# Kernel optimization log

Hardware: AMD Instinct MI355X
Metric: run time of the kernel (lower is better)

The kernel has to match this reference:

```python
import jax
import jax.numpy as jnp
from jax import lax
import numpy as np

EPS = 1e-5
CLASS_COUNT = 1000

# conv specs: (out_c, in_c, k, pool_stride)
_SPECS = [(8, 1, 11, 1), (32, 8, 7, 2), (64, 32, 5, 2), (64, 64, 5, 2), (128, 64, 5, 2), (128, 128, 3, 2)]


def _maxpool3(x, stride):
    return lax.reduce_window(x, -jnp.inf, lax.max, (1, 1, 3, 3), (1, 1, stride, stride), 'VALID')


def _block(x, w, gamma, beta, pool_stride):
    # tanh soft-binarized weights (mode=1, w=1)
    wq = jnp.tanh(w)
    y = lax.conv_general_dilated(x, wq, (1, 1), 'VALID', dimension_numbers=('NCHW', 'OIHW', 'NCHW'))
    y = _maxpool3(y, pool_stride)
    # BatchNorm2d in training mode: batch statistics over (N,H,W), biased var
    mu = jnp.mean(y, axis=(0, 2, 3), keepdims=True)
    var = jnp.var(y, axis=(0, 2, 3), keepdims=True)
    y = (y - mu) * lax.rsqrt(var + EPS)
    y = y * gamma.reshape(1, -1, 1, 1) + beta.reshape(1, -1, 1, 1)
    # tanh soft-binarized activation (mode=1, w=1)
    return jnp.tanh(y)


def setup_inputs() -> dict:
    key = jax.random.key(0)
    keys = jax.random.split(key, 8)
    inp = {'x': jax.random.normal(keys[0], (128, 1, 227, 227), dtype=jnp.float32)}
    for i, (oc, ic, k, _) in enumerate(_SPECS):
        fan_in = ic * k * k
        inp[f'w{i+1}'] = jax.random.normal(keys[i + 1], (oc, ic, k, k), dtype=jnp.float32) / np.sqrt(fan_in)
        inp[f'g{i+1}'] = jnp.ones((oc,), dtype=jnp.float32)
        inp[f'b{i+1}'] = jnp.zeros((oc,), dtype=jnp.float32)
    inp['wl'] = jax.random.normal(keys[7], (CLASS_COUNT, 512), dtype=jnp.float32) / np.sqrt(512.0)
    return inp


def reference(x, w1, w2, w3, w4, w5, w6, g1, g2, g3, g4, g5, g6,
              b1, b2, b3, b4, b5, b6, wl):
    ws = (w1, w2, w3, w4, w5, w6)
    gs = (g1, g2, g3, g4, g5, g6)
    bs = (b1, b2, b3, b4, b5, b6)
    for i, (_, _, _, ps) in enumerate(_SPECS):
        x = _block(x, ws[i], gs[i], bs[i], ps)
    # flatten -> BinaryLinear (tanh-binarized weight, no bias)
    x = x.reshape(x.shape[0], -1)  # [B, 512]
    return x @ jnp.tanh(wl).T  # [B, classCount]
```

## Files before the change

### kernel.cpp

```cpp
#include <hip/hip_runtime.h>
#include <hip/hip_bf16.h>
#include <hip/hip_fp16.h>

using bf16 = __hip_bfloat16;
using f16  = _Float16;
using f16x8 = __attribute__((ext_vector_type(8))) _Float16;
using f32x4  = __attribute__((ext_vector_type(4))) float;
typedef unsigned long long u64;

__device__ __forceinline__ float b2f(bf16 v){ return __bfloat162float(v); }
__device__ __forceinline__ bf16 f2b(float v){ return __float2bfloat16(v); }
__device__ __forceinline__ float ldf(const float* p){ return *p; }
__device__ __forceinline__ float ldf(const bf16* p){ return b2f(*p); }
__device__ __forceinline__ float ldf(const __half* p){ return __half2float(*p); }
__device__ __forceinline__ void stf(float* p, float v){ *p = v; }
__device__ __forceinline__ void stf(bf16* p, float v){ *p = f2b(v); }
__device__ __forceinline__ void stf(__half* p, float v){ *p = __float2half(v); }

__device__ __forceinline__ float ftanh(float x){
    float t = __builtin_amdgcn_exp2f(x * 2.8853900817779268f);
    return 1.0f - 2.0f * __builtin_amdgcn_rcpf(t + 1.0f);
}

__device__ __forceinline__ float ld_any(const void* p, int i, int isBf16)
{
    return isBf16 ? b2f(((const bf16*)p)[i]) : ((const float*)p)[i];
}

__device__ __forceinline__ int det_bf(const void* g)
{
    return (*(const unsigned*)g == 0x3F803F80u) ? 1 : 0;
}

__device__ __forceinline__ void bn_pr(const float* __restrict__ sums,
                                      const void* __restrict__ g,
                                      const void* __restrict__ b,
                                      int bf, int C, float inv, int c,
                                      float& sc, float& sh)
{
    float mean = sums[c] * inv;
    float var  = sums[C + c] * inv - mean * mean;
    float rstd = rsqrtf(fmaxf(var, 0.f) + 1e-5f);
    sc = ld_any(g, c, bf) * rstd;
    sh = ld_any(b, c, bf) - mean * sc;
}

__global__ __launch_bounds__(256)
void prep_all(const void* __restrict__ w1, const void* __restrict__ w6,
              const void* __restrict__ wlw, const void* __restrict__ w2,
              const void* __restrict__ w3, const void* __restrict__ w4,
              const void* __restrict__ w5, const void* __restrict__ g1,
              float* __restrict__ wq0, float* __restrict__ wq5,
              float* __restrict__ wlqT, __half* __restrict__ wpk,
              __half* __restrict__ wpk3, __half* __restrict__ wpk4,
              __half* __restrict__ wpk5, int* __restrict__ flag)
{
    const int bf = det_bf(g1);
    const int b = blockIdx.x, t = threadIdx.x;
    if (b == 0 && t == 0) *flag = bf;
    if (b < 4) {
        int i = b * 256 + t;
        if (i < 968) wq0[i] = tanhf(ld_any(w1, i, bf));
    } else if (b < 580) {
        int i = (b - 4) * 256 + t;
        if (i < 147456) wq5[i] = tanhf(ld_any(w6, i, bf));
    } else if (b < 2580) {
        int i = (b - 580) * 256 + t;
        if (i < 512000) {
            int cls = i >> 9, k = i & 511;
            wlqT[k * 1000 + cls] = tanhf(ld_any(wlw, i, bf));
        }
    } else if (b < 2636) {
        int i = (b - 2580) * 256 + t;
        if (i < 14336) {
            int ic  = i & 7;
            int q   = (i >> 3) & 3;
            int col = (i >> 5) & 15;
            int g   = (i >> 9) & 1;
            int khg = (i >> 10) & 1;
            int kw  = i >> 11;
            int kh  = khg * 4 + q;
            int oc  = g * 16 + col;
            __half v = __float2half(0.f);
            if (kh < 7)
                v = __float2half(tanhf(ld_any(w2, (oc * 8 + ic) * 49 + kh * 7 + kw, bf)));
            wpk[i] = v;
        }
    } else if (b < 2836) {
        int i = (b - 2636) * 256 + t;
        if (i < 51200) {
            int tap = i >> 11;
            int g   = (i >> 9) & 3;
            int col = (i >> 5) & 15;
            int icp = i & 31;
            int oc  = g * 16 + col;
            wpk3[i] = __float2half(tanhf(ld_any(w3, (oc * 32 + icp) * 25 + tap, bf)));
        }
    } else if (b < 3236) {
        int i = (b - 2836) * 256 + t;
        if (i < 102400) {
            int step = i >> 11;
            int g    = (i >> 9) & 3;
            int col  = (i >> 5) & 15;
            int icp  = i & 31;
            int icg  = step / 25, tap = step - icg * 25;
            int oc   = g * 16 + col;
            int ic   = icg * 32 + icp;
            wpk4[i] = __float2half(tanhf(ld_any(w4, (oc * 64 + ic) * 25 + tap, bf)));
        }
    } else {
        int i = (b - 3236) * 256 + t;
        if (i < 204800) {
            int step = i >> 12;
            int ocg  = (i >> 11) & 1;
            int g    = (i >> 9) & 3;
            int col  = (i >> 5) & 15;
            int icp  = i & 31;
            int icg  = step / 25, tap = step - icg * 25;
            int oc   = ocg * 64 + g * 16 + col;
            int ic   = icg * 32 + icp;
            wpk5[i] = __float2half(tanhf(ld_any(w5, (oc * 64 + ic) * 25 + tap, bf)));
        }
    }
}

__global__ __launch_bounds__(256)
void b2conv(const __half* __restrict__ A1, const __half* __restrict__ wpk,
            __half* __restrict__ raw, float* __restrict__ sums2,
            const float* __restrict__ sums1, const void* __restrict__ g1,
            const void* __restrict__ b1)
{
    __shared__ __align__(16) char smem[32000];
    __shared__ float s_part[512];
    f16*   xs = (f16*)smem;
    float* pb = (float*)smem;

    const int tid = threadIdx.x;
    const int n   = blockIdx.z;
    const int ty  = blockIdx.x / 15, tx = blockIdx.x - ty * 15;
    const int cy0 = ty * 30, cx0 = tx * 14;

    const int bf1 = det_bf(g1);
    float ssc[8], ssh[8];
    #pragma unroll
    for (int j = 0; j < 8; j++)
        bn_pr(sums1, g1, b1, bf1, 8, 1.f / 5916800.f, j, ssc[j], ssh[j]);

    for (int i = tid; i < 858; i += 256) {
        int r = i / 22, c = i - r * 22;
        int gr = cy0 + r, gc = cx0 + c;
        f16x8 v = (f16x8){0, 0, 0, 0, 0, 0, 0, 0};
        if (gr < 215 && gc < 215)
            v = *(const f16x8*)((const f16*)A1 + ((size_t)(n * 215 + gr) * 215 + gc) * 8);
        f16x8 o;
        #pragma unroll
        for (int j = 0; j < 8; j++)
            o[j] = (f16)ftanh(fmaf((float)v[j], ssc[j], ssh[j]));
        *(f16x8*)(xs + i * 8) = o;
    }
    __syncthreads();

    const int lane = tid & 63, wid = tid >> 6;
    const int col = lane & 15, q = lane >> 4;
    const int arow = q * 22;

    f32x4 acc[8][2];
    #pragma unroll
    for (int f = 0; f < 8; f++)
        #pragma unroll
        for (int g = 0; g < 2; g++)
            acc[f][g] = (f32x4){0.f, 0.f, 0.f, 0.f};

    const f16* wb = (const f16*)wpk + col * 32 + q * 8;
    f16x8 wc0 = *(const f16x8*)(wb);
    f16x8 wc1 = *(const f16x8*)(wb + 512);

    #pragma unroll
    for (int s = 0; s < 14; s++) {
        f16x8 wn0 = wc0, wn1 = wc1;
        if (s < 13) {
            const f16* wn = wb + (s + 1) * 1024;
            wn0 = *(const f16x8*)(wn);
            wn1 = *(const f16x8*)(wn + 512);
        }
        int kw = s >> 1, khg = s & 1;
        int aoffs = arow + khg * 88 + kw;
        #pragma unroll
        for (int f = 0; f < 8; f++) {
            int gi = (wid * 8 + f) * 22 + col + aoffs;
            f16x8 a = *(const f16x8*)(xs + gi * 8);
            acc[f][0] = __builtin_amdgcn_mfma_f32_16x16x32_f16(a, wc0, acc[f][0], 0, 0, 0);
            acc[f][1] = __builtin_amdgcn_mfma_f32_16x16x32_f16(a, wc1, acc[f][1], 0, 0, 0);
        }
        wc0 = wn0; wc1 = wn1;
    }
    __syncthreads();

    for (int h = 0; h < 2; h++) {
        #pragma unroll
        for (int f = 0; f < 8; f++) {
            int cr = wid * 8 + f;
            if (cr < 31)
                *(f32x4*)(pb + col * 500 + cr * 16 + q * 4) = acc[f][h];
        }
        __syncthreads();
        const int ocl = tid >> 4, slot = tid & 15;
        float sm = 0.f, sq = 0.f;
        for (int j = slot; j < 105; j += 16) {
            int py = j / 7, px = j - (j / 7) * 7;
            int gph = ty * 15 + py, gpw = tx * 7 + px;
            if (gph < 104 && gpw < 104) {
                const float* cp = pb + ocl * 500 + (2 * py) * 16 + 2 * px;
                float m = cp[0];
                #pragma unroll
                for (int dy = 0; dy < 3; dy++)
                    #pragma unroll
                    for (int dx = 0; dx < 3; dx++)
                        m = fmaxf(m, cp[dy * 16 + dx]);
                int oc = h * 16 + ocl;
                size_t oidx = ((size_t)(n * 104 + gph) * 104 + gpw) * 32 + oc;
                raw[oidx] = __float2half(m);
                sm += m; sq += m * m;
            }
        }
        s_part[tid] = sm; s_part[256 + tid] = sq;
        __syncthreads();
        if (tid < 16) {
            float a = 0.f, b = 0.f;
            #pragma unroll
            for (int t = 0; t < 16; t++) {
                a += s_part[tid * 16 + t];
                b += s_part[256 + tid * 16 + t];
            }
            atomicAdd(&sums2[h * 16 + tid],      a);
            atomicAdd(&sums2[32 + h * 16 + tid], b);
        }
        __syncthreads();
    }
}

__global__ __launch_bounds__(256)
void b3conv(const __half* __restrict__ A2, const __half* __restrict__ wpk3,
            __half* __restrict__ A3, float* __restrict__ sums3,
            const float* __restrict__ sums2, const void* __restrict__ g2,
            const void* __restrict__ b2)
{
    __shared__ __align__(16) char smem[32000];
    __shared__ float s_part[512];
    f16*   xs = (f16*)smem;
    float* pb = (float*)smem;

    const int tid = threadIdx.x;
    const int n   = blockIdx.z;
    const int ty  = blockIdx.x / 7, tx = blockIdx.x - ty * 7;
    const int y0  = ty * 14, x0 = tx * 14;

    if (tid < 32) {
        float sc, sh;
        bn_pr(sums2, g2, b2, det_bf(g2), 32, 1.f / 1384448.f, tid, sc, sh);
        s_part[tid] = sc; s_part[32 + tid] = sh;
    }
    __syncthreads();

    for (int i = tid; i < 1600; i += 256) {
        int pos = i >> 2, g8 = i & 3;
        int gy = y0 + pos / 20, gx = x0 + pos % 20;
        f16x8 v = *(const f16x8*)((const f16*)A2 +
                  ((size_t)(n * 104 + gy) * 104 + gx) * 32 + g8 * 8);
        int c0 = g8 * 8;
        f16x8 o;
        #pragma unroll
        for (int j = 0; j < 8; j++)
            o[j] = (f16)ftanh(fmaf((float)v[j], s_part[c0 + j], s_part[32 + c0 + j]));
        *(f16x8*)(xs + pos * 40 + g8 * 8) = o;
    }

    const int lane = tid & 63, wid = tid >> 6;
    const int col = lane & 15, q = lane >> 4;

    f32x4 acc[4][4];
    #pragma unroll
    for (int f = 0; f < 4; f++)
        #pragma unroll
        for (int g = 0; g < 4; g++)
            acc[f][g] = (f32x4){0.f, 0.f, 0.f, 0.f};

    const f16* wb = (const f16*)wpk3 + col * 32 + q * 8;
    f16x8 w[4];
    #pragma unroll
    for (int g = 0; g < 4; g++)
        w[g] = *(const f16x8*)(wb + g * 512);

    __syncthreads();

    #pragma unroll 1
    for (int tap = 0; tap < 25; tap++) {
        const f16* wnb = wb + (tap < 24 ? tap + 1 : tap) * 2048;
        f16x8 wn[4];
        #pragma unroll
        for (int g = 0; g < 4; g++)
            wn[g] = *(const f16x8*)(wnb + g * 512);

        int kh = tap / 5, kw = tap - (tap / 5) * 5;
        f16x8 a[4];
        #pragma unroll
        for (int f = 0; f < 4; f++) {
            int pos = (wid * 4 + f + kh) * 20 + col + kw;
            a[f] = *(const f16x8*)(xs + pos * 40 + q * 8);
        }
        #pragma unroll
        for (int g = 0; g < 4; g++)
            #pragma unroll
            for (int f = 0; f < 4; f++)
                acc[f][g] = __builtin_amdgcn_mfma_f32_16x16x32_f16(
                    a[f], w[g], acc[f][g], 0, 0, 0);
        #pragma unroll
        for (int g = 0; g < 4; g++)
            w[g] = wn[g];
    }

    for (int h = 0; h < 2; h++) {
        __syncthreads();
        #pragma unroll
        for (int f = 0; f < 4; f++) {
            int cr = wid * 4 + f;
            if (cr < 15) {
                #pragma unroll
                for (int gg = 0; gg < 2; gg++)
                    *(f32x4*)(pb + (gg * 16 + col) * 244 + cr * 16 + q * 4) = acc[f][h * 2 + gg];
            }
        }
        __syncthreads();
        const int ocl = tid >> 3, slot = tid & 7;
        float sm = 0.f, sq = 0.f;
        for (int j = slot; j < 49; j += 8) {
            int py = j / 7, px = j - (j / 7) * 7;
            const float* cp = pb + ocl * 244 + (2 * py) * 16 + 2 * px;
            float m = cp[0];
            #pragma unroll
            for (int dy = 0; dy < 3; dy++)
                #pragma unroll
                for (int dx = 0; dx < 3; dx++)
                    m = fmaxf(m, cp[dy * 16 + dx]);
            A3[((size_t)(n * 64 + h * 32 + ocl) * 49 + ty * 7 + py) * 49 + tx * 7 + px]
                = __float2half(m);
            sm += m; sq += m * m;
        }
        s_part[tid] = sm; s_part[256 + tid] = sq;
        __syncthreads();
        if (tid < 32) {
            float a = 0.f, b = 0.f;
            #pragma unroll
            for (int t = 0; t < 8; t++) {
                a += s_part[tid * 8 + t];
                b += s_part[256 + tid * 8 + t];
            }
            atomicAdd(&sums3[h * 32 + tid],      a);
            atomicAdd(&sums3[64 + h * 32 + tid], b);
        }
    }
}

__global__ __launch_bounds__(256)
void bn_tanh_h_t(const __half* __restrict__ x, __half* __restrict__ out,
                 const float* __restrict__ sums3, const void* __restrict__ g3,
                 const void* __restrict__ b3)
{
    __shared__ float tile[64][50];
    __shared__ float s_ss[128];
    const int tid = threadIdx.x;
    const int h = blockIdx.x % 49;
    const int n = blockIdx.x / 49;
    const int c = tid >> 2, j = tid & 3;
    if (tid < 64) {
        float sc, sh;
        bn_pr(sums3, g3, b3, det_bf(g3), 64, 1.f / 307328.f, tid, sc, sh);
        s_ss[tid] = sc; s_ss[64 + tid] = sh;
    }
    const __half* xp = x + ((size_t)(n * 64 + c) * 49 + h) * 49;
    for (int w = j; w < 49; w += 4)
        tile[c][w] = __half2float(xp[w]);
    __syncthreads();
    __half* op = out + ((size_t)(n * 49 + h) * 49) * 64;
    for (int pos = tid; pos < 49 * 64; pos += 256) {
        int w = pos >> 6, cc = pos & 63;
        op[pos] = __float2half(ftanh(fmaf(tile[cc][w], s_ss[cc], s_ss[64 + cc])));
    }
}

__global__ __launch_bounds__(256)
void bn4_apply(const __half* __restrict__ x, __half* __restrict__ out,
               const float* __restrict__ sums4, const void* __restrict__ g4,
               const void* __restrict__ b4)
{
    __shared__ float s_ss[128];
    int tid = threadIdx.x;
    if (tid < 64) {
        float sc, sh;
        bn_pr(sums4, g4, b4, det_bf(g4), 64, 1.f / 61952.f, tid, sc, sh);
        s_ss[tid] = sc; s_ss[64 + tid] = sh;
    }
    __syncthreads();
    int idx = blockIdx.x * 256 + tid;
    if (idx >= 3964928) return;
    int w  = idx % 22;
    int t1 = idx / 22;
    int h  = t1 % 22;
    int t2 = t1 / 22;
    int c  = t2 & 63;
    int n  = t2 >> 6;
    float t = ftanh(fmaf(__half2float(x[idx]), s_ss[c], s_ss[64 + c]));
    out[((size_t)(n * 22 + h) * 22 + w) * 64 + c] = __float2half(t);
}

__global__ __launch_bounds__(256)
void b4conv(const __half* __restrict__ A3t, const __half* __restrict__ wpk4,
            __half* __restrict__ A4, float* __restrict__ sums4)
{
    __shared__ __align__(16) char smem[31232];
    __shared__ float s_part[512];
    f16*   xs = (f16*)smem;
    float* pb = (float*)smem;

    const int tid = threadIdx.x;
    const int n   = blockIdx.z;
    const int ty  = blockIdx.x >> 2, tx = blockIdx.x & 3;
    const int y0  = ty * 14, x0 = tx * 14;
    const int lane = tid & 63, wid = tid >> 6;
    const int col = lane & 15, q = lane >> 4;

    f32x4 acc[4][4];
    #pragma unroll
    for (int f = 0; f < 4; f++)
        #pragma unroll
        for (int g = 0; g < 4; g++)
            acc[f][g] = (f32x4){0.f, 0.f, 0.f, 0.f};

    const f16* wb = (const f16*)wpk4 + col * 32 + q * 8;
    f16x8 w[4];
    #pragma unroll
    for (int g = 0; g < 4; g++)
        w[g] = *(const f16x8*)(wb + g * 512);

    #pragma unroll 1
    for (int icg = 0; icg < 2; icg++) {
        __syncthreads();
        for (int i = tid; i < 1520; i += 256) {
            int pos = i >> 2, g8 = i & 3;
            int gy = y0 + pos / 20, gx = x0 + pos % 20;
            f16x8 v = (f16x8){0, 0, 0, 0, 0, 0, 0, 0};
            if (gy < 49 && gx < 49)
                v = *(const f16x8*)((const f16*)A3t +
                    ((size_t)(n * 49 + gy) * 49 + gx) * 64 + icg * 32 + g8 * 8);
            *(f16x8*)(xs + pos * 40 + g8 * 8) = v;
        }
        __syncthreads();

        #pragma unroll 1
        for (int tap = 0; tap < 25; tap++) {
            int step = icg * 25 + tap;
            const f16* wnb = wb + (size_t)(step < 49 ? step + 1 : step) * 2048;
            f16x8 wn[4];
            #pragma unroll
            for (int g = 0; g < 4; g++)
                wn[g] = *(const f16x8*)(wnb + g * 512);

            int kh = tap / 5, kw = tap - (tap / 5) * 5;
            f16x8 a[4];
            #pragma unroll
            for (int f = 0; f < 4; f++) {
                int r = wid * 4 + f + kh; if (r > 18) r = 18;
                int pos = r * 20 + col + kw;
                a[f] = *(const f16x8*)(xs + pos * 40 + q * 8);
            }
            #pragma unroll
            for (int g = 0; g < 4; g++)
                #pragma unroll
                for (int f = 0; f < 4; f++)
                    acc[f][g] = __builtin_amdgcn_mfma_f32_16x16x32_f16(
                        a[f], w[g], acc[f][g], 0, 0, 0);
            #pragma unroll
            for (int g = 0; g < 4; g++)
                w[g] = wn[g];
        }
    }

    for (int h = 0; h < 2; h++) {
        __syncthreads();
        #pragma unroll
        for (int f = 0; f < 4; f++) {
            int cr = wid * 4 + f;
            if (cr < 15) {
                #pragma unroll
                for (int gg = 0; gg < 2; gg++)
                    *(f32x4*)(pb + (gg * 16 + col) * 244 + cr * 16 + q * 4) = acc[f][h * 2 + gg];
            }
        }
        __syncthreads();
        const int ocl = tid >> 3, slot = tid & 7;
        float sm = 0.f, sq = 0.f;
        for (int j = slot; j < 49; j += 8) {
            int py = j / 7, px = j - (j / 7) * 7;
            int gph = ty * 7 + py, gpw = tx * 7 + px;
            if (gph < 22 && gpw < 22) {
                const float* cp = pb + ocl * 244 + (2 * py) * 16 + 2 * px;
                float m = cp[0];
                #pragma unroll
                for (int dy = 0; dy < 3; dy++)
                    #pragma unroll
                    for (int dx = 0; dx < 3; dx++)
                        m = fmaxf(m, cp[dy * 16 + dx]);
                A4[((size_t)(n * 64 + h * 32 + ocl) * 22 + gph) * 22 + gpw]
                    = __float2half(m);
                sm += m; sq += m * m;
            }
        }
        s_part[tid] = sm; s_part[256 + tid] = sq;
        __syncthreads();
        if (tid < 32) {
            float a = 0.f, b = 0.f;
            #pragma unroll
            for (int t = 0; t < 8; t++) {
                a += s_part[tid * 8 + t];
                b += s_part[256 + tid * 8 + t];
            }
            atomicAdd(&sums4[h * 32 + tid],      a);
            atomicAdd(&sums4[64 + h * 32 + tid], b);
        }
    }
}

__global__ __launch_bounds__(256)
void b5conv(const __half* __restrict__ A4t, const __half* __restrict__ wpk5,
            float* __restrict__ A5, float* __restrict__ sums5)
{
    __shared__ __align__(16) char smem[49664];
    __shared__ float s_part[512];
    f16*   xs = (f16*)smem;
    float* pb = (float*)smem;

    const int tid = threadIdx.x;
    const int n   = blockIdx.z;
    const int ocg = blockIdx.x;
    const int lane = tid & 63, wid = tid >> 6;
    const int col = lane & 15, q = lane >> 4;

    int abase[6];
    #pragma unroll
    for (int f = 0; f < 6; f++) {
        int m = (wid * 6 + f) * 16 + col;
        if (m > 323) m = 323;
        int r = m / 18, cc = m - r * 18;
        abase[f] = r * 22 + cc;
    }

    f32x4 acc[6][4];
    #pragma unroll
    for (int f = 0; f < 6; f++)
        #pragma unroll
        for (int g = 0; g < 4; g++)
            acc[f][g] = (f32x4){0.f, 0.f, 0.f, 0.f};

    const f16* wb = (const f16*)wpk5 + ocg * 2048 + col * 32 + q * 8;
    f16x8 w[4];
    #pragma unroll
    for (int g = 0; g < 4; g++)
        w[g] = *(const f16x8*)(wb + g * 512);

    #pragma unroll 1
    for (int icg = 0; icg < 2; icg++) {
        __syncthreads();
        for (int i = tid; i < 1936; i += 256) {
            int pos = i >> 2, g8 = i & 3;
            *(f16x8*)(xs + pos * 40 + g8 * 8) =
                *(const f16x8*)((const f16*)A4t + ((size_t)(n * 484 + pos)) * 64
                                + icg * 32 + g8 * 8);
        }
        __syncthreads();

        #pragma unroll 1
        for (int tap = 0; tap < 25; tap++) {
            int step = icg * 25 + tap;
            const f16* wnb = wb + (size_t)(step < 49 ? step + 1 : step) * 4096;
            f16x8 wn[4];
            #pragma unroll
            for (int g = 0; g < 4; g++)
                wn[g] = *(const f16x8*)(wnb + g * 512);

            int kh = tap / 5, kw = tap - (tap / 5) * 5;
            int off = kh * 22 + kw;
            f16x8 a[6];
            #pragma unroll
            for (int f = 0; f < 6; f++)
                a[f] = *(const f16x8*)(xs + (abase[f] + off) * 40 + q * 8);
            #pragma unroll
            for (int g = 0; g < 4; g++)
                #pragma unroll
                for (int f = 0; f < 6; f++)
                    acc[f][g] = __builtin_amdgcn_mfma_f32_16x16x32_f16(
                        a[f], w[g], acc[f][g], 0, 0, 0);
            #pragma unroll
            for (int g = 0; g < 4; g++)
                w[g] = wn[g];
        }
    }

    for (int h = 0; h < 2; h++) {
        __syncthreads();
        #pragma unroll
        for (int f = 0; f < 6; f++)
            #pragma unroll
            for (int gg = 0; gg < 2; gg++)
                *(f32x4*)(pb + (gg * 16 + col) * 388 + (wid * 6 + f) * 16 + q * 4)
                    = acc[f][h * 2 + gg];
        __syncthreads();
        const int ocl = tid >> 3, slot = tid & 7;
        float sm = 0.f, sq = 0.f;
        for (int j = slot; j < 64; j += 8) {
            int py = j >> 3, px = j & 7;
            const float* cp = pb + ocl * 388 + (2 * py) * 18 + 2 * px;
            float m = cp[0];
            #pragma unroll
            for (int dy = 0; dy < 3; dy++)
                #pragma unroll
                for (int dx = 0; dx < 3; dx++)
                    m = fmaxf(m, cp[dy * 18 + dx]);
            int oc = ocg * 64 + h * 32 + ocl;
            A5[((size_t)(n * 128 + oc) * 8 + py) * 8 + px] = m;
            sm += m; sq += m * m;
        }
        s_part[tid] = sm; s_part[256 + tid] = sq;
        __syncthreads();
        if (tid < 32) {
            float a = 0.f, b = 0.f;
            #pragma unroll
            for (int t = 0; t < 8; t++) {
                a += s_part[tid * 8 + t];
                b += s_part[256 + tid * 8 + t];
            }
            int oc = ocg * 64 + h * 32 + tid;
            atomicAdd(&sums5[oc],       a);
            atomicAdd(&sums5[128 + oc], b);
        }
    }
}

template<int MODE, int RAWIN, int IC, int OC, int K, int PS, int TPH, int TPW,
         int OCB, int OCT, int CIC, int NP, bool ONHWC, typename InT, typename OutT>
__global__ __launch_bounds__(256)
void ctile(const void* __restrict__ in, const float* __restrict__ wq,
           OutT* __restrict__ out, float* __restrict__ sums,
           const float* __restrict__ ss, const void* __restrict__ g1in,
           int Hin, int Win, int PH, int PW, int tilesX)
{
    constexpr int TPO  = OCB / OCT;
    constexpr int CH   = PS * (TPH - 1) + 3;
    constexpr int CW   = PS * (TPW - 1) + 3;
    constexpr int SPR  = (CW + NP - 1) / NP;
    constexpr int CWP  = SPR * NP;
    constexpr int NSTR = CH * SPR;
    static_assert(NSTR * TPO <= 256, "thread mapping overflow");
    constexpr int IH   = CH + K - 1;
    constexpr int IW   = CW + K - 1;
    constexpr int IWE_ = (CWP + K - 1 > IW) ? (CWP + K - 1) : IW;
    constexpr int IWE  = IWE_ | 1;
    constexpr int IN_SZ  = CIC * IH * IWE;
    constexpr int INP    = (IN_SZ + 3) & ~3;
    constexpr int W_SZ   = CIC * K * K * OCB;
    constexpr int CONV_SZ = OCB * CH * CWP;
    constexpr int LDS_SZ = (INP + W_SZ > CONV_SZ) ? (INP + W_SZ) : CONV_SZ;

    __shared__ __align__(16) float lds[LDS_SZ];
    __shared__ float s_part[512];

    const int tid = threadIdx.x;
    const int n   = blockIdx.z;
    const int oc0 = blockIdx.y * OCB;
    const int tY  = blockIdx.x / tilesX;
    const int tX  = blockIdx.x - tY * tilesX;
    const int ph0 = tY * TPH, pw0 = tX * TPW;
    const int ih0 = ph0 * PS, iw0 = pw0 * PS;

    const int bfin = RAWIN ? det_bf(g1in) : 0;

    const int  og  = tid % TPO;
    const int  s   = tid / TPO;
    const bool act = (s < NSTR);
    const int  r   = s / SPR;
    const int  c0  = (s - r * SPR) * NP;

    float acc[NP][OCT];
    #pragma unroll
    for (int p = 0; p < NP; p++)
        #pragma unroll
        for (int o = 0; o < OCT; o++) acc[p][o] = 0.f;

    for (int icb = 0; icb < IC; icb += CIC) {
        for (int idx = tid; idx < IN_SZ; idx += 256) {
            int ic  = idx / (IH * IWE);
            int rem = idx - ic * (IH * IWE);
            int rr  = rem / IWE, cc = rem - rr * IWE;
            int gr  = ih0 + rr, gc = iw0 + cc;
            float v = 0.f;
            if (gr < Hin && gc < Win) {
                size_t gidx = ((size_t)(n * IC + icb + ic) * Hin + gr) * Win + gc;
                v = RAWIN ? ld_any(in, (int)gidx, bfin) : ldf(&((const InT*)in)[gidx]);
            }
            lds[idx] = v;
        }
        for (int idx = tid; idx < W_SZ; idx += 256) {
            int ocl = idx % OCB;
            int kk  = (idx / OCB) % (K * K);
            int c_  = idx / (OCB * K * K);
            lds[INP + idx] = wq[((size_t)(oc0 + ocl) * IC + icb + c_) * (K * K) + kk];
        }
        __syncthreads();

        if (act) {
            #pragma unroll 1
            for (int ic_ = 0; ic_ < CIC; ic_++) {
                const float* xb = lds + ic_ * (IH * IWE);
                const float* wb = lds + INP + ic_ * (K * K * OCB) + og * OCT;
                #pragma unroll 1
                for (int kh = 0; kh < K; kh++) {
                    const float* xr = xb + (r + kh) * IWE + c0;
                    float xwin[NP + K - 1];
                    #pragma unroll
                    for (int j = 0; j < NP + K - 1; j++) xwin[j] = xr[j];
                    #pragma unroll
                    for (int kw = 0; kw < K; kw++) {
                        const float* wp2 = wb + (kh * K + kw) * OCB;
                        float wv[OCT];
                        #pragma unroll
                        for (int o = 0; o < OCT; o += 4) {
                            float4 t = *(const float4*)(wp2 + o);
                            wv[o] = t.x; wv[o+1] = t.y; wv[o+2] = t.z; wv[o+3] = t.w;
                        }
                        #pragma unroll
                        for (int p = 0; p < NP; p++)
                            #pragma unroll
                            for (int o = 0; o < OCT; o++)
                                acc[p][o] = fmaf(wv[o], xwin[p + kw], acc[p][o]);
                    }
                }
            }
        }
        __syncthreads();
    }

    if (act) {
        #pragma unroll
        for (int p = 0; p < NP; p++)
            #pragma unroll
            for (int o = 0; o < OCT; o++)
                lds[(og * OCT + o) * (CH * CWP) + r * CWP + c0 + p] = acc[p][o];
    }
    __syncthreads();

    {
        constexpr int TPC = 256 / OCB;
        const int ocl = tid / TPC, slot = tid - ocl * TPC;
        float sm = 0.f, sq = 0.f;
        for (int j = slot; j < TPH * TPW; j += TPC) {
            int py = j / TPW, px = j - (j / TPW) * TPW;
            int gph = ph0 + py, gpw = pw0 + px;
            if (gph < PH && gpw < PW) {
                const float* cp = lds + ocl * (CH * CWP) + (py * PS) * CWP + px * PS;
                float m = cp[0];
                #pragma unroll
                for (int dy = 0; dy < 3; dy++)
                    #pragma unroll
                    for (int dx = 0; dx < 3; dx++)
                        m = fmaxf(m, cp[dy * CWP + dx]);
                size_t oidx = ONHWC
                    ? ((size_t)(n * PH + gph) * PW + gpw) * OC + oc0 + ocl
                    : ((size_t)(n * OC + oc0 + ocl) * PH + gph) * PW + gpw;
                if (MODE == 2) {
                    int c = oc0 + ocl;
                    stf(&out[oidx], ftanh(fmaf(m, ss[c], ss[OC + c])));
                } else {
                    if (MODE == 0) stf(&out[oidx], m);
                    sm += m; sq += m * m;
                }
            }
        }
        if (MODE != 2) {
            s_part[tid] = sm; s_part[256 + tid] = sq;
            __syncthreads();
            if (tid < OCB) {
                float a = 0.f, b = 0.f;
                #pragma unroll
                for (int t = 0; t < TPC; t++) {
                    a += s_part[tid * TPC + t];
                    b += s_part[256 + tid * TPC + t];
                }
                atomicAdd(&sums[oc0 + tid],      a);
                atomicAdd(&sums[OC + oc0 + tid], b);
            }
        }
    }
}

template<int K, int APPLY, typename InT, typename OutT>
__global__ __launch_bounds__(256)
void convpool(const InT* __restrict__ in, const float* __restrict__ wq,
              OutT* __restrict__ out, const float* __restrict__ ss,
              int IC, int OC, int PS, int Hin, int Win, int PH, int PW, int total)
{
    for (int idx = blockIdx.x * 256 + threadIdx.x; idx < total;
         idx += gridDim.x * 256) {
        int pw = idx % PW;
        int t1 = idx / PW;
        int ph = t1 % PH;
        int t2 = t1 / PH;
        int oc = t2 % OC;
        int n  = t2 / OC;
        const int by = ph * PS, bx = pw * PS;

        float acc[3][3];
        #pragma unroll
        for (int a = 0; a < 3; a++)
            #pragma unroll
            for (int b = 0; b < 3; b++) acc[a][b] = 0.f;

        const float* wp = wq + oc * IC * K * K;
        const InT*   np = in + (n * IC) * Hin * Win;

        #pragma unroll 1
        for (int ic = 0; ic < IC; ic++) {
            const InT*   xp = np + ic * Hin * Win;
            const float* wc = wp + ic * K * K;
            #pragma unroll
            for (int r = 0; r < K + 2; r++) {
                float xr[K + 2];
                const InT* xrow = xp + (by + r) * Win + bx;
                #pragma unroll
                for (int j = 0; j < K + 2; j++) xr[j] = ldf(&xrow[j]);
                #pragma unroll
                for (int dy = 0; dy < 3; dy++) {
                    const int kh = r - dy;
                    if (0 <= kh && kh < K) {
                        const float* wrow = wc + kh * K;
                        #pragma unroll
                        for (int kw = 0; kw < K; kw++) {
                            float w = wrow[kw];
                            acc[dy][0] = fmaf(w, xr[kw + 0], acc[dy][0]);
                            acc[dy][1] = fmaf(w, xr[kw + 1], acc[dy][1]);
                            acc[dy][2] = fmaf(w, xr[kw + 2], acc[dy][2]);
                        }
                    }
                }
            }
        }
        float m = acc[0][0];
        #pragma unroll
        for (int a = 0; a < 3; a++)
            #pragma unroll
            for (int b = 0; b < 3; b++) m = fmaxf(m, acc[a][b]);
        if (APPLY) m = ftanh(fmaf(m, ss[oc], ss[OC + oc]));
        stf(&out[idx], m);
    }
}

template<typename T>
__global__ __launch_bounds__(256)
void stats_k(const T* __restrict__ x, float* __restrict__ sums,
             int N, int C, int PHW, int bpc)
{
    int c   = blockIdx.x / bpc;
    int sub = blockIdx.x % bpc;
    int perC = N * PHW;
    float s = 0.f, s2 = 0.f;
    for (int j = sub * 256 + threadIdx.x; j < perC; j += bpc * 256) {
        int n = j / PHW, p = j - n * PHW;
        float v = ldf(&x[(n * C + c) * PHW + p]);
        s += v; s2 += v * v;
    }
    __shared__ float ls[256], ls2[256];
    ls[threadIdx.x] = s; ls2[threadIdx.x] = s2;
    __syncthreads();
    for (int w = 128; w > 0; w >>= 1) {
        if (threadIdx.x < w) {
            ls[threadIdx.x]  += ls[threadIdx.x + w];
            ls2[threadIdx.x] += ls2[threadIdx.x + w];
        }
        __syncthreads();
    }
    if (threadIdx.x == 0) {
        atomicAdd(&sums[c],     ls[0]);
        atomicAdd(&sums[C + c], ls2[0]);
    }
}

__global__ __launch_bounds__(256)
void bn_tanh_p(float* __restrict__ x, const float* __restrict__ sums,
               const void* __restrict__ g, const void* __restrict__ b,
               int C, int PHW, float invCnt)
{
    int plane = blockIdx.y;
    int c = plane & (C - 1);
    float sc, sh;
    bn_pr(sums, g, b, det_bf(g), C, invCnt, c, sc, sh);
    float* xp = x + (long)plane * PHW;
    for (int i = blockIdx.x * 256 + threadIdx.x; i < PHW; i += 256 * gridDim.x)
        xp[i] = ftanh(fmaf(xp[i], sc, sh));
}

__global__ __launch_bounds__(256)
void linear_k(const float* __restrict__ act, const float* __restrict__ wlqT,
              void* __restrict__ out, const int* __restrict__ flag)
{
    __shared__ float s_a[512];
    int bf = *flag;
    int n = blockIdx.y;
    for (int i = threadIdx.x; i < 512; i += 256) s_a[i] = act[n * 512 + i];
    __syncthreads();
    int cls = blockIdx.x * 256 + threadIdx.x;
    if (cls < 1000) {
        float acc = 0.f;
        #pragma unroll 8
        for (int k = 0; k < 512; k++)
            acc = fmaf(s_a[k], wlqT[k * 1000 + cls], acc);
        if (bf) ((bf16*)out)[n * 1000 + cls] = f2b(acc);
        else    ((float*)out)[n * 1000 + cls] = acc;
    }
}

extern "C" void kernel_launch(void* const* d_in, const int* in_sizes, int n_in,
                              void* d_out, int out_size, void* d_ws, size_t ws_size,
                              hipStream_t stream)
{
    (void)in_sizes; (void)n_in; (void)out_size; (void)ws_size;
    const void* x = d_in[0];
    const void* W[6]; const void* G[6]; const void* B[6];
    for (int i = 0; i < 6; i++) {
        W[i] = d_in[1 + 3 * i];
        G[i] = d_in[2 + 3 * i];
        B[i] = d_in[3 + 3 * i];
    }
    const void* wl = d_in[19];

    char* p = (char*)d_ws;
    auto carve = [&](size_t bytes) -> void* {
        void* r = (void*)p;
        p += (bytes + 255) & ~((size_t)255);
        return r;
    };
    int*   flag = (int*)carve(256);
    const int wsz[6] = {968, 12544, 51200, 102400, 204800, 147456};
    float* wq[6];
    for (int i = 0; i < 6; i++) wq[i] = (float*)carve((size_t)wsz[i] * 4);
    float* wlqT = (float*)carve((size_t)512000 * 4);
    float* sums_all = (float*)carve(1536 * 4);
    float* S1 = sums_all;        float* S2 = sums_all + 256;
    float* S3 = sums_all + 512;  float* S4 = sums_all + 768;
    float* S5 = sums_all + 1024; float* S6 = sums_all + 1280;
    __half* wpk  = (__half*)carve((size_t)14336 * 2);
    __half* wpk3 = (__half*)carve((size_t)51200 * 2);
    __half* wpk4 = (__half*)carve((size_t)102400 * 2);
    __half* wpk5 = (__half*)carve((size_t)204800 * 2);
    __half* A1  = (__half*)carve((size_t)47334400 * 2);
    __half* A2  = (__half*)carve((size_t)44302336 * 2);
    __half* A3  = (__half*)A1;
    __half* A3t = (__half*)A2;
    __half* A4  = (__half*)A1;
    float*  A5  = (float*)A2;
    __half* A4t = (__half*)((char*)A2 + (size_t)16 * 1024 * 1024);
    float*  A6  = (float*)A1;

    auto cdiv = [](int a, int b) { return (a + b - 1) / b; };

    hipMemsetAsync(sums_all, 0, 1536 * 4, stream);
    prep_all<<<4036, 256, 0, stream>>>(W[0], W[5], wl, W[1], W[2], W[3], W[4], G[0],
                                       wq[0], wq[5], wlqT, wpk, wpk3, wpk4, wpk5, flag);

    ctile<0, 1, 1, 8, 11, 1, 34, 40, 8, 8, 1, 7, true, float, __half>
        <<<dim3(42, 1, 128), 256, 0, stream>>>(x, wq[0], A1, S1, S1, G[0], 227, 227, 215, 215, 6);

    b2conv<<<dim3(105, 1, 128), 256, 0, stream>>>(A1, wpk, A2, S2, S1, G[0], B[0]);

    b3conv<<<dim3(49, 1, 128), 256, 0, stream>>>(A2, wpk3, A3, S3, S2, G[1], B[1]);
    bn_tanh_h_t<<<128 * 49, 256, 0, stream>>>(A3, A3t, S3, G[2], B[2]);

    b4conv<<<dim3(16, 1, 128), 256, 0, stream>>>(A3t, wpk4, A4, S4);
    bn4_apply<<<cdiv(3964928, 256), 256, 0, stream>>>(A4, A4t, S4, G[3], B[3]);

    b5conv<<<dim3(2, 1, 128), 256, 0, stream>>>(A4t, wpk5, A5, S5);
    bn_tanh_p<<<dim3(1, 16384), 256, 0, stream>>>(A5, S5, G[4], B[4], 128, 64, 1.f / 8192.f);

    {
        int total = 65536;
        convpool<3, 0, float, float><<<cdiv(total, 256), 256, 0, stream>>>(
            A5, wq[5], A6, S6, 128, 128, 2, 8, 8, 2, 2, total);
        stats_k<float><<<128, 256, 0, stream>>>(A6, S6, 128, 128, 4, 1);
        bn_tanh_p<<<dim3(1, 16384), 256, 0, stream>>>(A6, S6, G[5], B[5], 128, 4, 1.f / 512.f);
    }
    linear_k<<<dim3(4, 128), 256, 0, stream>>>(A6, wlqT, d_out, flag);
}
```

Baseline: 1.342 ms.

## Fuse BN+tanh for blocks 3 and 4 into next conv's input staging

```diff
diff --git a/kernel.cpp b/kernel.cpp
--- a/kernel.cpp
+++ b/kernel.cpp
@@ -241,7 +241,7 @@
 
 __global__ __launch_bounds__(256)
 void b3conv(const __half* __restrict__ A2, const __half* __restrict__ wpk3,
-            __half* __restrict__ A3, float* __restrict__ sums3,
+            __half* __restrict__ A3t, float* __restrict__ sums3,
             const float* __restrict__ sums2, const void* __restrict__ g2,
             const void* __restrict__ b2)
 {
@@ -342,7 +342,8 @@
                 #pragma unroll
                 for (int dx = 0; dx < 3; dx++)
                     m = fmaxf(m, cp[dy * 16 + dx]);
-            A3[((size_t)(n * 64 + h * 32 + ocl) * 49 + ty * 7 + py) * 49 + tx * 7 + px]
+            int gph = ty * 7 + py, gpw = tx * 7 + px;
+            A3t[((size_t)(n * 49 + gph) * 49 + gpw) * 64 + h * 32 + ocl]
                 = __float2half(m);
             sm += m; sq += m * m;
         }
@@ -362,63 +363,14 @@
 }
 
 __global__ __launch_bounds__(256)
-void bn_tanh_h_t(const __half* __restrict__ x, __half* __restrict__ out,
-                 const float* __restrict__ sums3, const void* __restrict__ g3,
-                 const void* __restrict__ b3)
-{
-    __shared__ float tile[64][50];
-    __shared__ float s_ss[128];
-    const int tid = threadIdx.x;
-    const int h = blockIdx.x % 49;
-    const int n = blockIdx.x / 49;
-    const int c = tid >> 2, j = tid & 3;
-    if (tid < 64) {
-        float sc, sh;
-        bn_pr(sums3, g3, b3, det_bf(g3), 64, 1.f / 307328.f, tid, sc, sh);
-        s_ss[tid] = sc; s_ss[64 + tid] = sh;
-    }
-    const __half* xp = x + ((size_t)(n * 64 + c) * 49 + h) * 49;
-    for (int w = j; w < 49; w += 4)
-        tile[c][w] = __half2float(xp[w]);
-    __syncthreads();
-    __half* op = out + ((size_t)(n * 49 + h) * 49) * 64;
-    for (int pos = tid; pos < 49 * 64; pos += 256) {
-        int w = pos >> 6, cc = pos & 63;
-        op[pos] = __float2half(ftanh(fmaf(tile[cc][w], s_ss[cc], s_ss[64 + cc])));
-    }
-}
-
-__global__ __launch_bounds__(256)
-void bn4_apply(const __half* __restrict__ x, __half* __restrict__ out,
-               const float* __restrict__ sums4, const void* __restrict__ g4,
-               const void* __restrict__ b4)
-{
-    __shared__ float s_ss[128];
-    int tid = threadIdx.x;
-    if (tid < 64) {
-        float sc, sh;
-        bn_pr(sums4, g4, b4, det_bf(g4), 64, 1.f / 61952.f, tid, sc, sh);
-        s_ss[tid] = sc; s_ss[64 + tid] = sh;
-    }
-    __syncthreads();
-    int idx = blockIdx.x * 256 + tid;
-    if (idx >= 3964928) return;
-    int w  = idx % 22;
-    int t1 = idx / 22;
-    int h  = t1 % 22;
-    int t2 = t1 / 22;
-    int c  = t2 & 63;
-    int n  = t2 >> 6;
-    float t = ftanh(fmaf(__half2float(x[idx]), s_ss[c], s_ss[64 + c]));
-    out[((size_t)(n * 22 + h) * 22 + w) * 64 + c] = __float2half(t);
-}
-
-__global__ __launch_bounds__(256)
 void b4conv(const __half* __restrict__ A3t, const __half* __restrict__ wpk4,
-            __half* __restrict__ A4, float* __restrict__ sums4)
+            __half* __restrict__ A4, float* __restrict__ sums4,
+            const float* __restrict__ sums3, const void* __restrict__ g3,
+            const void* __restrict__ b3)
 {
     __shared__ __align__(16) char smem[31232];
     __shared__ float s_part[512];
+    __shared__ float s_ss[128];
     f16*   xs = (f16*)smem;
     float* pb = (float*)smem;
 
@@ -429,6 +381,12 @@
     const int lane = tid & 63, wid = tid >> 6;
     const int col = lane & 15, q = lane >> 4;
 
+    if (tid < 64) {
+        float sc, sh;
+        bn_pr(sums3, g3, b3, det_bf(g3), 64, 1.f / 307328.f, tid, sc, sh);
+        s_ss[tid] = sc; s_ss[64 + tid] = sh;
+    }
+
     f32x4 acc[4][4];
     #pragma unroll
     for (int f = 0; f < 4; f++)
@@ -448,11 +406,16 @@
         for (int i = tid; i < 1520; i += 256) {
             int pos = i >> 2, g8 = i & 3;
             int gy = y0 + pos / 20, gx = x0 + pos % 20;
-            f16x8 v = (f16x8){0, 0, 0, 0, 0, 0, 0, 0};
-            if (gy < 49 && gx < 49)
-                v = *(const f16x8*)((const f16*)A3t +
+            f16x8 o = (f16x8){0, 0, 0, 0, 0, 0, 0, 0};
+            if (gy < 49 && gx < 49) {
+                f16x8 v = *(const f16x8*)((const f16*)A3t +
                     ((size_t)(n * 49 + gy) * 49 + gx) * 64 + icg * 32 + g8 * 8);
-            *(f16x8*)(xs + pos * 40 + g8 * 8) = v;
+                int c0 = icg * 32 + g8 * 8;
+                #pragma unroll
+                for (int j = 0; j < 8; j++)
+                    o[j] = (f16)ftanh(fmaf((float)v[j], s_ss[c0 + j], s_ss[64 + c0 + j]));
+            }
+            *(f16x8*)(xs + pos * 40 + g8 * 8) = o;
         }
         __syncthreads();
 
@@ -510,7 +473,7 @@
                     #pragma unroll
                     for (int dx = 0; dx < 3; dx++)
                         m = fmaxf(m, cp[dy * 16 + dx]);
-                A4[((size_t)(n * 64 + h * 32 + ocl) * 22 + gph) * 22 + gpw]
+                A4[((size_t)(n * 22 + gph) * 22 + gpw) * 64 + h * 32 + ocl]
                     = __float2half(m);
                 sm += m; sq += m * m;
             }
@@ -531,11 +494,14 @@
 }
 
 __global__ __launch_bounds__(256)
-void b5conv(const __half* __restrict__ A4t, const __half* __restrict__ wpk5,
-            float* __restrict__ A5, float* __restrict__ sums5)
+void b5conv(const __half* __restrict__ A4, const __half* __restrict__ wpk5,
+            float* __restrict__ A5, float* __restrict__ sums5,
+            const float* __restrict__ sums4, const void* __restrict__ g4,
+            const void* __restrict__ b4)
 {
     __shared__ __align__(16) char smem[49664];
     __shared__ float s_part[512];
+    __shared__ float s_ss[128];
     f16*   xs = (f16*)smem;
     float* pb = (float*)smem;
 
@@ -545,6 +511,12 @@
     const int lane = tid & 63, wid = tid >> 6;
     const int col = lane & 15, q = lane >> 4;
 
+    if (tid < 64) {
+        float sc, sh;
+        bn_pr(sums4, g4, b4, det_bf(g4), 64, 1.f / 61952.f, tid, sc, sh);
+        s_ss[tid] = sc; s_ss[64 + tid] = sh;
+    }
+
     int abase[6];
     #pragma unroll
     for (int f = 0; f < 6; f++) {
@@ -572,9 +544,14 @@
         __syncthreads();
         for (int i = tid; i < 1936; i += 256) {
             int pos = i >> 2, g8 = i & 3;
-            *(f16x8*)(xs + pos * 40 + g8 * 8) =
-                *(const f16x8*)((const f16*)A4t + ((size_t)(n * 484 + pos)) * 64
-                                + icg * 32 + g8 * 8);
+            f16x8 v = *(const f16x8*)((const f16*)A4 + ((size_t)(n * 484 + pos)) * 64
+                                      + icg * 32 + g8 * 8);
+            int c0 = icg * 32 + g8 * 8;
+            f16x8 o;
+            #pragma unroll
+            for (int j = 0; j < 8; j++)
+                o[j] = (f16)ftanh(fmaf((float)v[j], s_ss[c0 + j], s_ss[64 + c0 + j]));
+            *(f16x8*)(xs + pos * 40 + g8 * 8) = o;
         }
         __syncthreads();
 
@@ -959,14 +936,14 @@
     __half* wpk3 = (__half*)carve((size_t)51200 * 2);
     __half* wpk4 = (__half*)carve((size_t)102400 * 2);
     __half* wpk5 = (__half*)carve((size_t)204800 * 2);
-    __half* A1  = (__half*)carve((size_t)47334400 * 2);
-    __half* A2  = (__half*)carve((size_t)44302336 * 2);
-    __half* A3  = (__half*)A1;
-    __half* A3t = (__half*)A2;
-    __half* A4  = (__half*)A1;
-    float*  A5  = (float*)A2;
-    __half* A4t = (__half*)((char*)A2 + (size_t)16 * 1024 * 1024);
-    float*  A6  = (float*)A1;
+    __half* R1  = (__half*)carve((size_t)47334400 * 2);
+    __half* R2  = (__half*)carve((size_t)44302336 * 2);
+    __half* A1  = R1;
+    __half* A2  = R2;
+    __half* A3t = R1;
+    __half* A4  = R2;
+    float*  A5  = (float*)R1;
+    float*  A6  = (float*)R2;
 
     auto cdiv = [](int a, int b) { return (a + b - 1) / b; };
 
@@ -979,13 +956,11 @@
 
     b2conv<<<dim3(105, 1, 128), 256, 0, stream>>>(A1, wpk, A2, S2, S1, G[0], B[0]);
 
-    b3conv<<<dim3(49, 1, 128), 256, 0, stream>>>(A2, wpk3, A3, S3, S2, G[1], B[1]);
-    bn_tanh_h_t<<<128 * 49, 256, 0, stream>>>(A3, A3t, S3, G[2], B[2]);
-
-    b4conv<<<dim3(16, 1, 128), 256, 0, stream>>>(A3t, wpk4, A4, S4);
-    bn4_apply<<<cdiv(3964928, 256), 256, 0, stream>>>(A4, A4t, S4, G[3], B[3]);
-
-    b5conv<<<dim3(2, 1, 128), 256, 0, stream>>>(A4t, wpk5, A5, S5);
+    b3conv<<<dim3(49, 1, 128), 256, 0, stream>>>(A2, wpk3, A3t, S3, S2, G[1], B[1]);
+
+    b4conv<<<dim3(16, 1, 128), 256, 0, stream>>>(A3t, wpk4, A4, S4, S3, G[2], B[2]);
+
+    b5conv<<<dim3(2, 1, 128), 256, 0, stream>>>(A4, wpk5, A5, S5, S4, G[3], B[3]);
     bn_tanh_p<<<dim3(1, 16384), 256, 0, stream>>>(A5, S5, G[4], B[4], 128, 64, 1.f / 8192.f);
 
     {
```

Result: faster. 1.305 ms (-2.7%).
